# Performance work log

Hardware: AMD Instinct MI355X
Metric: run time of the kernel (lower is better)

Reference implementation:

```python
import jax, jax.numpy as jnp
import numpy as np

B, TQ, TM, D, ATTN, H = 8, 1024, 1024, 512, 512, 8
HEAD_DIM = ATTN // H
TEMPERATURE = 1.0
CAUSALITY = True
NEG_INF = -2.0 ** 32 + 1


def setup_inputs() -> dict:
    key = jax.random.key(0)
    ks = jax.random.split(key, 7)
    scale = 1.0 / np.sqrt(D)
    return {
        "inputs": jax.random.normal(ks[0], (B, TQ, D), dtype=jnp.float32),
        "memory": jax.random.normal(ks[1], (B, TM, D), dtype=jnp.float32),
        "Wq": jax.random.normal(ks[2], (D, ATTN), dtype=jnp.float32) * scale,
        "Wk": jax.random.normal(ks[3], (D, ATTN), dtype=jnp.float32) * scale,
        "Wv": jax.random.normal(ks[4], (D, ATTN), dtype=jnp.float32) * scale,
        "memory_lengths": jax.random.randint(ks[5], (B,), TM // 2, TM + 1, dtype=jnp.int32),
        "query_lengths": jax.random.randint(ks[6], (B,), TQ // 2, TQ + 1, dtype=jnp.int32),
    }


def _split_head(x):
    # [B, T, ATTN] -> [B, H, T, HEAD_DIM]
    b, t, _ = x.shape
    return x.reshape(b, t, H, HEAD_DIM).transpose(0, 2, 1, 3)


def reference(inputs, memory, Wq, Wk, Wv, memory_lengths, query_lengths):
    q = _split_head(inputs @ Wq)   # [B,H,Tq,hd]
    k = _split_head(memory @ Wk)   # [B,H,Tm,hd]
    v = _split_head(memory @ Wv)   # [B,H,Tm,hd]

    logits = jnp.einsum("bhqd,bhmd->bhqm", q, k)
    logits = logits / jnp.sqrt(jnp.float32(HEAD_DIM)) / TEMPERATURE

    mem_mask = jnp.arange(TM)[None, :] < memory_lengths[:, None]   # [B,Tm]
    qry_mask = jnp.arange(TQ)[None, :] < query_lengths[:, None]    # [B,Tq]
    length_mask = qry_mask[:, :, None] & mem_mask[:, None, :]      # [B,Tq,Tm]
    mask = length_mask[:, None, :, :]                              # [B,1,Tq,Tm]
    if CAUSALITY:
        causal = jnp.tril(jnp.ones((TQ, TM), dtype=bool))
        mask = mask & causal[None, None, :, :]

    logits = jnp.where(mask, logits, jnp.float32(NEG_INF))
    alignments = jax.nn.softmax(logits, axis=3)                    # [B,H,Tq,Tm]
    contexts = jnp.einsum("bhqm,bhmd->bhqd", alignments, v)
    contexts = contexts.transpose(0, 2, 1, 3).reshape(inputs.shape[0], TQ, ATTN)
    return contexts, alignments
```

## Files before the change

kernel.cpp:

```cpp
#include <hip/hip_runtime.h>

#define NB 8
#define NTQ 1024
#define NTM 1024
#define ND 512
#define NATTN 512
#define NH 8
#define NDH 64

typedef _Float16 half8 __attribute__((ext_vector_type(8)));
typedef float f32x4 __attribute__((ext_vector_type(4)));

__global__ __launch_bounds__(256) void proj_kernel(
    const float* __restrict__ inputs, const float* __restrict__ memory,
    const float* __restrict__ Wq, const float* __restrict__ Wk,
    const float* __restrict__ Wv,
    _Float16* __restrict__ Qh, _Float16* __restrict__ Kh,
    _Float16* __restrict__ Vth) {
  const int z = blockIdx.z;
  const float* __restrict__ A = (z == 0) ? inputs : memory;
  const float* __restrict__ W = (z == 0) ? Wq : ((z == 1) ? Wk : Wv);
  const int row0 = blockIdx.y * 64;
  const int col0 = blockIdx.x * 64;

  __shared__ __align__(16) _Float16 As[64][72];
  __shared__ __align__(16) _Float16 Wt[64][72];

  const int t = threadIdx.x;
  const int w = t >> 6;
  const int L = t & 63;
  const int lrow = L & 15;
  const int quad = L >> 4;
  const int sr = t >> 2;
  const int sc = (t & 3) * 16;

  const f32x4 zf = {0.f, 0.f, 0.f, 0.f};
  f32x4 acc[4];
#pragma unroll
  for (int i = 0; i < 4; i++) acc[i] = zf;

  for (int k0 = 0; k0 < ND; k0 += 64) {
    {
      const float4* src = (const float4*)(A + (size_t)(row0 + sr) * ND + k0 + sc);
      float4 f0 = src[0], f1 = src[1], f2 = src[2], f3 = src[3];
      half8 h0, h1;
      h0[0] = (_Float16)f0.x; h0[1] = (_Float16)f0.y; h0[2] = (_Float16)f0.z; h0[3] = (_Float16)f0.w;
      h0[4] = (_Float16)f1.x; h0[5] = (_Float16)f1.y; h0[6] = (_Float16)f1.z; h0[7] = (_Float16)f1.w;
      h1[0] = (_Float16)f2.x; h1[1] = (_Float16)f2.y; h1[2] = (_Float16)f2.z; h1[3] = (_Float16)f2.w;
      h1[4] = (_Float16)f3.x; h1[5] = (_Float16)f3.y; h1[6] = (_Float16)f3.z; h1[7] = (_Float16)f3.w;
      *(half8*)&As[sr][sc] = h0;
      *(half8*)&As[sr][sc + 8] = h1;
    }
    {
      const float4* src = (const float4*)(W + (size_t)(k0 + sr) * NATTN + col0 + sc);
      float4 g0 = src[0], g1 = src[1], g2 = src[2], g3 = src[3];
      float gv[16];
      *(float4*)&gv[0] = g0; *(float4*)&gv[4] = g1;
      *(float4*)&gv[8] = g2; *(float4*)&gv[12] = g3;
#pragma unroll
      for (int j = 0; j < 16; j++) Wt[sc + j][sr] = (_Float16)gv[j];
    }
    __syncthreads();
#pragma unroll
    for (int ks = 0; ks < 2; ks++) {
      half8 a = *(const half8*)&As[w * 16 + lrow][ks * 32 + quad * 8];
#pragma unroll
      for (int nt = 0; nt < 4; nt++) {
        half8 b = *(const half8*)&Wt[nt * 16 + lrow][ks * 32 + quad * 8];
        acc[nt] = __builtin_amdgcn_mfma_f32_16x16x32_f16(a, b, acc[nt], 0, 0, 0);
      }
    }
    __syncthreads();
  }

  const int b = row0 >> 10;
  const int tr0 = row0 & 1023;
  const int hh = col0 >> 6;
  if (z <= 1) {
    _Float16* dst = (z == 0 ? Qh : Kh) + (size_t)(b * NH + hh) * NTQ * NDH;
#pragma unroll
    for (int nt = 0; nt < 4; nt++) {
#pragma unroll
      for (int r = 0; r < 4; r++) {
        int trow = tr0 + w * 16 + quad * 4 + r;
        int d = nt * 16 + lrow;
        dst[(size_t)trow * NDH + d] = (_Float16)acc[nt][r];
      }
    }
  } else {
#pragma unroll
    for (int nt = 0; nt < 4; nt++) {
#pragma unroll
      for (int r = 0; r < 4; r++)
        As[nt * 16 + lrow][w * 16 + quad * 4 + r] = (_Float16)acc[nt][r];
    }
    __syncthreads();
    _Float16* dst = Vth + ((size_t)(b * NH + hh) * NDH + sr) * NTM + tr0 + sc;
    *(half8*)dst = *(const half8*)&As[sr][sc];
    *(half8*)(dst + 8) = *(const half8*)&As[sr][sc + 8];
  }
}

__global__ __launch_bounds__(256) void attn_kernel(
    const _Float16* __restrict__ Qh, const _Float16* __restrict__ Kh,
    const _Float16* __restrict__ Vth, const int* __restrict__ mem_len,
    const int* __restrict__ qry_len, float* __restrict__ ctx_out,
    float* __restrict__ align_out) {
  const int bh = blockIdx.x;
  const int qt = blockIdx.y;
  const int bb = bh >> 3;
  const int hh = bh & 7;
  const int q0 = qt * 64;

  __shared__ __align__(16) _Float16 Qs[64][72];
  __shared__ __align__(16) _Float16 Ks[64][72];
  __shared__ __align__(16) _Float16 Vts[64][72];
  __shared__ __align__(16) _Float16 Ps[4][16][72];

  const int t = threadIdx.x, w = t >> 6, L = t & 63;
  const int lrow = L & 15, quad = L >> 4;
  const int qlen = qry_len[bb], mlen = mem_len[bb];
  const int mtop = (mlen + 63) >> 6;
  const int n_comp = (q0 + 63 >= qlen) ? 16 : min(qt + 1, mtop);
  const _Float16* Qbase = Qh + (size_t)bh * NTQ * NDH;
  const _Float16* Kbase = Kh + (size_t)bh * NTM * NDH;
  const _Float16* Vbase = Vth + (size_t)bh * NDH * NTM;
  const int sr = t >> 2, sc = (t & 3) * 16;
  const f32x4 zf = {0.f, 0.f, 0.f, 0.f};
  float* abase = align_out + (size_t)bh * NTQ * NTM;

  if (n_comp < 16) {
    const int c0 = n_comp * 64;
    float* rp = abase + (size_t)(q0 + sr) * NTM;
    const float4 z4 = {0.f, 0.f, 0.f, 0.f};
    for (int c = c0 + (t & 3) * 4; c < NTM; c += 16) *(float4*)(rp + c) = z4;
  }

  {
    const half8* src = (const half8*)(Qbase + (size_t)(q0 + sr) * NDH + sc);
    *(half8*)&Qs[sr][sc] = src[0];
    *(half8*)&Qs[sr][sc + 8] = src[1];
  }
  const int qg = q0 + w * 16 + quad * 4;
  float rowsum[4] = {0.f, 0.f, 0.f, 0.f};
  __syncthreads();

  for (int mt = 0; mt < n_comp; mt++) {
    {
      const half8* src = (const half8*)(Kbase + (size_t)(mt * 64 + sr) * NDH + sc);
      *(half8*)&Ks[sr][sc] = src[0];
      *(half8*)&Ks[sr][sc + 8] = src[1];
    }
    __syncthreads();
    f32x4 sacc[4];
#pragma unroll
    for (int i = 0; i < 4; i++) sacc[i] = zf;
#pragma unroll
    for (int ks = 0; ks < 2; ks++) {
      half8 a = *(const half8*)&Qs[w * 16 + lrow][ks * 32 + quad * 8];
#pragma unroll
      for (int nt = 0; nt < 4; nt++) {
        half8 b = *(const half8*)&Ks[nt * 16 + lrow][ks * 32 + quad * 8];
        sacc[nt] = __builtin_amdgcn_mfma_f32_16x16x32_f16(a, b, sacc[nt], 0, 0, 0);
      }
    }
#pragma unroll
    for (int nt = 0; nt < 4; nt++) {
      int m = mt * 64 + nt * 16 + lrow;
#pragma unroll
      for (int r = 0; r < 4; r++) {
        int q = qg + r;
        float p;
        if (q >= qlen) p = 1.0f;
        else if (m > q || m >= mlen) p = 0.0f;
        else p = __expf(sacc[nt][r] * 0.125f);
        rowsum[r] += p;
      }
    }
    __syncthreads();
  }
  float inv[4];
#pragma unroll
  for (int r = 0; r < 4; r++) {
    float s = rowsum[r];
    s += __shfl_xor(s, 1, 16);
    s += __shfl_xor(s, 2, 16);
    s += __shfl_xor(s, 4, 16);
    s += __shfl_xor(s, 8, 16);
    inv[r] = 1.0f / s;
  }

  f32x4 cacc[4];
#pragma unroll
  for (int i = 0; i < 4; i++) cacc[i] = zf;

  for (int mt = 0; mt < n_comp; mt++) {
    {
      const half8* src = (const half8*)(Kbase + (size_t)(mt * 64 + sr) * NDH + sc);
      *(half8*)&Ks[sr][sc] = src[0];
      *(half8*)&Ks[sr][sc + 8] = src[1];
      const half8* vsrc = (const half8*)(Vbase + (size_t)sr * NTM + mt * 64 + sc);
      *(half8*)&Vts[sr][sc] = vsrc[0];
      *(half8*)&Vts[sr][sc + 8] = vsrc[1];
    }
    __syncthreads();
    f32x4 sacc[4];
#pragma unroll
    for (int i = 0; i < 4; i++) sacc[i] = zf;
#pragma unroll
    for (int ks = 0; ks < 2; ks++) {
      half8 a = *(const half8*)&Qs[w * 16 + lrow][ks * 32 + quad * 8];
#pragma unroll
      for (int nt = 0; nt < 4; nt++) {
        half8 b = *(const half8*)&Ks[nt * 16 + lrow][ks * 32 + quad * 8];
        sacc[nt] = __builtin_amdgcn_mfma_f32_16x16x32_f16(a, b, sacc[nt], 0, 0, 0);
      }
    }
#pragma unroll
    for (int nt = 0; nt < 4; nt++) {
      int m = mt * 64 + nt * 16 + lrow;
#pragma unroll
      for (int r = 0; r < 4; r++) {
        int q = qg + r;
        float p;
        if (q >= qlen) p = inv[r];
        else if (m > q || m >= mlen) p = 0.0f;
        else p = __expf(sacc[nt][r] * 0.125f) * inv[r];
        abase[(size_t)q * NTM + m] = p;
        Ps[w][quad * 4 + r][nt * 16 + lrow] = (_Float16)p;
      }
    }
#pragma unroll
    for (int ks = 0; ks < 2; ks++) {
      half8 a = *(const half8*)&Ps[w][lrow][ks * 32 + quad * 8];
#pragma unroll
      for (int dt = 0; dt < 4; dt++) {
        half8 b = *(const half8*)&Vts[dt * 16 + lrow][ks * 32 + quad * 8];
        cacc[dt] = __builtin_amdgcn_mfma_f32_16x16x32_f16(a, b, cacc[dt], 0, 0, 0);
      }
    }
    __syncthreads();
  }

  float* cbase = ctx_out + (size_t)bb * NTQ * NATTN + (size_t)hh * NDH;
#pragma unroll
  for (int dt = 0; dt < 4; dt++) {
#pragma unroll
    for (int r = 0; r < 4; r++) {
      int q = qg + r;
      cbase[(size_t)q * NATTN + dt * 16 + lrow] = cacc[dt][r];
    }
  }
}

extern "C" void kernel_launch(void* const* d_in, const int* in_sizes, int n_in,
                              void* d_out, int out_size, void* d_ws,
                              size_t ws_size, hipStream_t stream) {
  const float* inputs = (const float*)d_in[0];
  const float* memory = (const float*)d_in[1];
  const float* Wq = (const float*)d_in[2];
  const float* Wk = (const float*)d_in[3];
  const float* Wv = (const float*)d_in[4];
  const int* mlen = (const int*)d_in[5];
  const int* qlen = (const int*)d_in[6];

  float* ctx = (float*)d_out;
  float* align = ctx + (size_t)NB * NTQ * NATTN;

  _Float16* Qh = (_Float16*)d_ws;
  _Float16* Kh = Qh + (size_t)NB * NH * NTQ * NDH;
  _Float16* Vth = Kh + (size_t)NB * NH * NTM * NDH;

  proj_kernel<<<dim3(8, 128, 3), 256, 0, stream>>>(inputs, memory, Wq, Wk, Wv,
                                                   Qh, Kh, Vth);
  attn_kernel<<<dim3(64, 16), 256, 0, stream>>>(Qh, Kh, Vth, mlen, qlen, ctx,
                                                align);
}
```

Measured before the change: 418.7 us.

## Pre-transpose weights to fp16 and widen projection tiles with XCD-aware mapping

Adds a prep kernel that converts the Q/K/V weights to fp16 and transposes them once, staging the result in the alignment output buffer as scratch before attention overwrites it. The projection kernel now computes 64x128 tiles, loading weights as vectorized fp16 rows instead of converting and transposing them per tile, and uses a 1D grid mapped so that each XCD handles contiguous row blocks. Q/K outputs are restaged through shared memory for vectorized stores. This adds a kernel launch and relies on the output buffer being free to use as scratch.

```diff
diff --git a/kernel.cpp b/kernel.cpp
--- a/kernel.cpp
+++ b/kernel.cpp
@@ -11,33 +11,59 @@
 typedef _Float16 half8 __attribute__((ext_vector_type(8)));
 typedef float f32x4 __attribute__((ext_vector_type(4)));
 
+__global__ __launch_bounds__(256) void wprep_kernel(
+    const float* __restrict__ Wq, const float* __restrict__ Wk,
+    const float* __restrict__ Wv, _Float16* __restrict__ Wt) {
+  const int z = blockIdx.z;
+  const float* __restrict__ W = (z == 0) ? Wq : ((z == 1) ? Wk : Wv);
+  _Float16* __restrict__ out = Wt + (size_t)z * NATTN * ND;
+  const int k0 = blockIdx.x * 64;
+  const int n0 = blockIdx.y * 64;
+  __shared__ __align__(16) _Float16 Ls[64][72];
+  const int t = threadIdx.x;
+  const int sr = t >> 2, sc = (t & 3) * 16;
+  const float4* src = (const float4*)(W + (size_t)(k0 + sr) * NATTN + n0 + sc);
+  float4 f0 = src[0], f1 = src[1], f2 = src[2], f3 = src[3];
+  float gv[16];
+  *(float4*)&gv[0] = f0; *(float4*)&gv[4] = f1;
+  *(float4*)&gv[8] = f2; *(float4*)&gv[12] = f3;
+#pragma unroll
+  for (int j = 0; j < 16; j++) Ls[sc + j][sr] = (_Float16)gv[j];
+  __syncthreads();
+  _Float16* dst = out + (size_t)(n0 + sr) * ND + k0 + sc;
+  *(half8*)dst = *(const half8*)&Ls[sr][sc];
+  *(half8*)(dst + 8) = *(const half8*)&Ls[sr][sc + 8];
+}
+
 __global__ __launch_bounds__(256) void proj_kernel(
     const float* __restrict__ inputs, const float* __restrict__ memory,
-    const float* __restrict__ Wq, const float* __restrict__ Wk,
-    const float* __restrict__ Wv,
-    _Float16* __restrict__ Qh, _Float16* __restrict__ Kh,
-    _Float16* __restrict__ Vth) {
-  const int z = blockIdx.z;
+    const _Float16* __restrict__ Wt, _Float16* __restrict__ Qh,
+    _Float16* __restrict__ Kh, _Float16* __restrict__ Vth) {
+  const int id = blockIdx.x;
+  const int xcd = id & 7;
+  const int g = id >> 3;
+  const int z = g >> 6;
+  const int gg = g & 63;
+  const int row0 = (xcd * 16 + (gg >> 2)) * 64;
+  const int col0 = (gg & 3) * 128;
+
   const float* __restrict__ A = (z == 0) ? inputs : memory;
-  const float* __restrict__ W = (z == 0) ? Wq : ((z == 1) ? Wk : Wv);
-  const int row0 = blockIdx.y * 64;
-  const int col0 = blockIdx.x * 64;
-
-  __shared__ __align__(16) _Float16 As[64][72];
-  __shared__ __align__(16) _Float16 Wt[64][72];
+  const _Float16* __restrict__ Wz = Wt + (size_t)z * NATTN * ND;
+
+  __shared__ __align__(16) _Float16 pool[64 * 72 + 128 * 72];
+  _Float16* Asb = pool;
+  _Float16* Wsb = pool + 64 * 72;
 
   const int t = threadIdx.x;
-  const int w = t >> 6;
-  const int L = t & 63;
-  const int lrow = L & 15;
-  const int quad = L >> 4;
-  const int sr = t >> 2;
-  const int sc = (t & 3) * 16;
+  const int w = t >> 6, L = t & 63;
+  const int lrow = L & 15, quad = L >> 4;
+  const int sr = t >> 2, sc = (t & 3) * 16;
+  const int sr2 = t >> 1, sc2 = (t & 1) * 32;
 
   const f32x4 zf = {0.f, 0.f, 0.f, 0.f};
-  f32x4 acc[4];
-#pragma unroll
-  for (int i = 0; i < 4; i++) acc[i] = zf;
+  f32x4 acc[8];
+#pragma unroll
+  for (int i = 0; i < 8; i++) acc[i] = zf;
 
   for (int k0 = 0; k0 < ND; k0 += 64) {
     {
@@ -48,56 +74,57 @@
       h0[4] = (_Float16)f1.x; h0[5] = (_Float16)f1.y; h0[6] = (_Float16)f1.z; h0[7] = (_Float16)f1.w;
       h1[0] = (_Float16)f2.x; h1[1] = (_Float16)f2.y; h1[2] = (_Float16)f2.z; h1[3] = (_Float16)f2.w;
       h1[4] = (_Float16)f3.x; h1[5] = (_Float16)f3.y; h1[6] = (_Float16)f3.z; h1[7] = (_Float16)f3.w;
-      *(half8*)&As[sr][sc] = h0;
-      *(half8*)&As[sr][sc + 8] = h1;
+      *(half8*)&Asb[sr * 72 + sc] = h0;
+      *(half8*)&Asb[sr * 72 + sc + 8] = h1;
     }
     {
-      const float4* src = (const float4*)(W + (size_t)(k0 + sr) * NATTN + col0 + sc);
-      float4 g0 = src[0], g1 = src[1], g2 = src[2], g3 = src[3];
-      float gv[16];
-      *(float4*)&gv[0] = g0; *(float4*)&gv[4] = g1;
-      *(float4*)&gv[8] = g2; *(float4*)&gv[12] = g3;
-#pragma unroll
-      for (int j = 0; j < 16; j++) Wt[sc + j][sr] = (_Float16)gv[j];
+      const half8* wsrc = (const half8*)(Wz + (size_t)(col0 + sr2) * ND + k0 + sc2);
+#pragma unroll
+      for (int j = 0; j < 4; j++) *(half8*)&Wsb[sr2 * 72 + sc2 + 8 * j] = wsrc[j];
     }
     __syncthreads();
 #pragma unroll
     for (int ks = 0; ks < 2; ks++) {
-      half8 a = *(const half8*)&As[w * 16 + lrow][ks * 32 + quad * 8];
-#pragma unroll
-      for (int nt = 0; nt < 4; nt++) {
-        half8 b = *(const half8*)&Wt[nt * 16 + lrow][ks * 32 + quad * 8];
+      half8 a = *(const half8*)&Asb[(w * 16 + lrow) * 72 + ks * 32 + quad * 8];
+#pragma unroll
+      for (int nt = 0; nt < 8; nt++) {
+        half8 b = *(const half8*)&Wsb[(nt * 16 + lrow) * 72 + ks * 32 + quad * 8];
         acc[nt] = __builtin_amdgcn_mfma_f32_16x16x32_f16(a, b, acc[nt], 0, 0, 0);
       }
     }
     __syncthreads();
   }
 
-  const int b = row0 >> 10;
+  const int bb = row0 >> 10;
   const int tr0 = row0 & 1023;
-  const int hh = col0 >> 6;
+  const int hh0 = col0 >> 6;
+
   if (z <= 1) {
-    _Float16* dst = (z == 0 ? Qh : Kh) + (size_t)(b * NH + hh) * NTQ * NDH;
-#pragma unroll
-    for (int nt = 0; nt < 4; nt++) {
-#pragma unroll
-      for (int r = 0; r < 4; r++) {
-        int trow = tr0 + w * 16 + quad * 4 + r;
-        int d = nt * 16 + lrow;
-        dst[(size_t)trow * NDH + d] = (_Float16)acc[nt][r];
-      }
-    }
+#pragma unroll
+    for (int nt = 0; nt < 8; nt++)
+#pragma unroll
+      for (int r = 0; r < 4; r++)
+        pool[(w * 16 + quad * 4 + r) * 136 + nt * 16 + lrow] = (_Float16)acc[nt][r];
+    __syncthreads();
+    const int sce = (t & 3) * 32;
+    _Float16* base = (z == 0) ? Qh : Kh;
+    _Float16* dst = base + (size_t)(bb * NH + hh0 + (sce >> 6)) * NTQ * NDH +
+                    (size_t)(tr0 + sr) * NDH + (sce & 63);
+#pragma unroll
+    for (int j = 0; j < 4; j++)
+      *(half8*)(dst + 8 * j) = *(const half8*)&pool[sr * 136 + sce + 8 * j];
   } else {
 #pragma unroll
-    for (int nt = 0; nt < 4; nt++) {
+    for (int nt = 0; nt < 8; nt++)
 #pragma unroll
       for (int r = 0; r < 4; r++)
-        As[nt * 16 + lrow][w * 16 + quad * 4 + r] = (_Float16)acc[nt][r];
-    }
-    __syncthreads();
-    _Float16* dst = Vth + ((size_t)(b * NH + hh) * NDH + sr) * NTM + tr0 + sc;
-    *(half8*)dst = *(const half8*)&As[sr][sc];
-    *(half8*)(dst + 8) = *(const half8*)&As[sr][sc + 8];
+        Wsb[(nt * 16 + lrow) * 72 + w * 16 + quad * 4 + r] = (_Float16)acc[nt][r];
+    __syncthreads();
+    _Float16* dst = Vth +
+        ((size_t)(bb * NH + hh0 + (sr2 >> 6)) * NDH + (sr2 & 63)) * NTM + tr0 + sc2;
+#pragma unroll
+    for (int j = 0; j < 4; j++)
+      *(half8*)(dst + 8 * j) = *(const half8*)&Wsb[sr2 * 72 + sc2 + 8 * j];
   }
 }
 
@@ -270,9 +297,10 @@
   _Float16* Qh = (_Float16*)d_ws;
   _Float16* Kh = Qh + (size_t)NB * NH * NTQ * NDH;
   _Float16* Vth = Kh + (size_t)NB * NH * NTM * NDH;
-
-  proj_kernel<<<dim3(8, 128, 3), 256, 0, stream>>>(inputs, memory, Wq, Wk, Wv,
-                                                   Qh, Kh, Vth);
+  _Float16* Wt = (_Float16*)align;
+
+  wprep_kernel<<<dim3(8, 8, 3), 256, 0, stream>>>(Wq, Wk, Wv, Wt);
+  proj_kernel<<<dim3(1536), 256, 0, stream>>>(inputs, memory, Wt, Qh, Kh, Vth);
   attn_kernel<<<dim3(64, 16), 256, 0, stream>>>(Qh, Kh, Vth, mlen, qlen, ctx,
                                                 align);
 }
```

After: 393.0 us. 6.1% less time.
